# Optimization experiments

Hardware: AMD Instinct MI355X
Metric: run time of the kernel (lower is better)

Reference implementation:

```python
import jax, jax.numpy as jnp
import numpy as np

N = 50000
E = 800000
EPS = 1e-5


def layer_norm(h, g, b):
    m = jnp.mean(h, axis=-1, keepdims=True)
    v = jnp.mean((h - m) ** 2, axis=-1, keepdims=True)
    return (h - m) * jax.lax.rsqrt(v + EPS) * g + b


def gcn_conv(x, src, dst, w, W, b):
    # PyG GCNConv: add self-loops (weight 1), symmetric normalization,
    # linear transform, scatter-add aggregation at dst, plus bias.
    n = x.shape[0]
    loop = jnp.arange(n)
    s = jnp.concatenate([src, loop])
    d = jnp.concatenate([dst, loop])
    wf = jnp.concatenate([w, jnp.ones((n,), dtype=x.dtype)])
    deg = jax.ops.segment_sum(wf, d, num_segments=n)
    dinv = jnp.where(deg > 0, deg, 1.0) ** -0.5
    dinv = jnp.where(deg > 0, dinv, 0.0)
    norm = dinv[s] * wf * dinv[d]            # [E+N]
    h = x @ W                                 # [N, out]
    msg = h[s] * norm[:, None]                # gather + scale
    out = jax.ops.segment_sum(msg, d, num_segments=n)  # scatter-add
    return out + b


def setup_inputs() -> dict:
    key = jax.random.key(0)
    ks = jax.random.split(key, 16)
    din, dh, dout = 128, 128, 64
    p = lambda k, shp: jax.random.normal(k, shp, dtype=jnp.float32) * 0.05
    return {
        "x": jax.random.normal(ks[0], (N, din), dtype=jnp.float32),
        "edge_index": jax.random.randint(ks[1], (2, E), 0, N),
        "edge_weight": jax.random.uniform(ks[2], (E,), dtype=jnp.float32),
        "W1": p(ks[3], (din, dh)), "b1": jnp.zeros((dh,), jnp.float32),
        "g1": jnp.ones((dh,), jnp.float32), "t1": jnp.zeros((dh,), jnp.float32),
        "W2": p(ks[4], (dh, dh)), "b2": jnp.zeros((dh,), jnp.float32),
        "g2": jnp.ones((dh,), jnp.float32), "t2": jnp.zeros((dh,), jnp.float32),
        "W3": p(ks[5], (dh, dout)), "b3": jnp.zeros((dout,), jnp.float32),
        "g3": jnp.ones((dout,), jnp.float32), "t3": jnp.zeros((dout,), jnp.float32),
    }


def reference(x, edge_index, edge_weight, W1, b1, g1, t1, W2, b2, g2, t2, W3, b3, g3, t3):
    src, dst = edge_index[0], edge_index[1]
    h = gcn_conv(x, src, dst, edge_weight, W1, b1)
    h = jax.nn.relu(layer_norm(h, g1, t1))
    h = gcn_conv(h, src, dst, edge_weight, W2, b2)
    h = jax.nn.relu(layer_norm(h, g2, t2))
    h = gcn_conv(h, src, dst, edge_weight, W3, b3)
    h = layer_norm(h, g3, t3)  # last layer: no relu/dropout
    return h
```

## Files before the change

kernel.cpp:

```cpp
#include <hip/hip_runtime.h>


typedef __attribute__((ext_vector_type(8))) short short8;
typedef __attribute__((ext_vector_type(4))) float f32x4;

static constexpr float FXS  = 16777216.0f;
static constexpr float FXSI = 1.0f / 16777216.0f;

__device__ __forceinline__ unsigned short f2bf(float f) {
    unsigned int u = __float_as_uint(f);
    u += 0x7FFFu + ((u >> 16) & 1u);
    return (unsigned short)(u >> 16);
}
__device__ __forceinline__ float bflo(unsigned int w) { return __uint_as_float(w << 16); }
__device__ __forceinline__ float bfhi(unsigned int w) { return __uint_as_float(w & 0xFFFF0000u); }

__device__ __forceinline__ void accum8(float* acc, const uint4 w, float nr) {
    acc[0] = fmaf(bflo(w.x), nr, acc[0]); acc[1] = fmaf(bfhi(w.x), nr, acc[1]);
    acc[2] = fmaf(bflo(w.y), nr, acc[2]); acc[3] = fmaf(bfhi(w.y), nr, acc[3]);
    acc[4] = fmaf(bflo(w.z), nr, acc[4]); acc[5] = fmaf(bfhi(w.z), nr, acc[5]);
    acc[6] = fmaf(bflo(w.w), nr, acc[6]); acc[7] = fmaf(bfhi(w.w), nr, acc[7]);
}

__global__ __launch_bounds__(256) void prep_kernel(
    const int* __restrict__ dst, const float* __restrict__ ew,
    unsigned long long* __restrict__ packed, int* __restrict__ rank, int nE, int eb4,
    const float* __restrict__ X, unsigned short* __restrict__ Xb, int total4, int xbk,
    const float* __restrict__ W1, const float* __restrict__ W2,
    const float* __restrict__ W3, unsigned short* __restrict__ Wt1,
    unsigned short* __restrict__ Wt2, unsigned short* __restrict__ Wt3)
{
    const int b = blockIdx.x;
    if (b < eb4) {
        const int e0 = b * 1024 + threadIdx.x;
        int   d[4]; float w[4]; bool v[4];
#pragma unroll
        for (int u = 0; u < 4; ++u) {
            const int e = e0 + u * 256;
            v[u] = e < nE;
            if (v[u]) { d[u] = dst[e]; w[u] = ew[e]; }
        }
        unsigned long long old[4];
#pragma unroll
        for (int u = 0; u < 4; ++u)
            if (v[u]) {
                const unsigned long long fx =
                    (unsigned long long)__float2uint_rn(w[u] * FXS);
                old[u] = atomicAdd(&packed[d[u]], (1ULL << 40) | fx);
            }
#pragma unroll
        for (int u = 0; u < 4; ++u)
            if (v[u]) rank[e0 + u * 256] = (int)(old[u] >> 40);
    } else if (b < eb4 + xbk) {
        const int i = (b - eb4) * 256 + threadIdx.x;
        if (i < total4) {
            const float4 v = ((const float4*)X)[i];
            ushort4 o;
            o.x = f2bf(v.x); o.y = f2bf(v.y); o.z = f2bf(v.z); o.w = f2bf(v.w);
            ((ushort4*)Xb)[i] = o;
        }
    } else {
        const int i = (b - eb4 - xbk) * 256 + threadIdx.x;
        if (i < 16384) {
            const int j = i >> 7, k = i & 127;
            Wt1[i] = f2bf(W1[k * 128 + j]);
        } else if (i < 32768) {
            const int q = i - 16384, j = q >> 7, k = q & 127;
            Wt2[q] = f2bf(W2[k * 128 + j]);
        } else if (i < 40960) {
            const int q = i - 32768, j = q >> 7, k = q & 127;
            Wt3[q] = f2bf(W3[k * 64 + j]);
        }
    }
}

__global__ __launch_bounds__(256) void dinv_partial_kernel(
    const unsigned long long* __restrict__ packed, int* __restrict__ partials,
    float* __restrict__ dinv, int n)
{
    const int b = blockIdx.x;
    const int i = b * 256 + threadIdx.x;
    int c = 0;
    if (i < n) {
        const unsigned long long p = packed[i];
        c = (int)(p >> 40);
        const float deg = (float)(p & ((1ULL << 40) - 1)) * FXSI;
        dinv[i] = rsqrtf(deg + 1.0f);
    }
#pragma unroll
    for (int off = 32; off; off >>= 1) c += __shfl_xor(c, off);
    __shared__ int red[4];
    if ((threadIdx.x & 63) == 0) red[threadIdx.x >> 6] = c;
    __syncthreads();
    if (threadIdx.x == 0) partials[b] = red[0] + red[1] + red[2] + red[3];
}

__global__ __launch_bounds__(256) void scanp_kernel(
    int* __restrict__ partials, int* __restrict__ rowptr, int n, int nblk)
{
    __shared__ int buf[256];
    const int v = (threadIdx.x < nblk) ? partials[threadIdx.x] : 0;
    buf[threadIdx.x] = v;
    __syncthreads();
    for (int off = 1; off < 256; off <<= 1) {
        const int t = (threadIdx.x >= off) ? buf[threadIdx.x - off] : 0;
        __syncthreads();
        buf[threadIdx.x] += t;
        __syncthreads();
    }
    if (threadIdx.x < nblk) partials[threadIdx.x] = buf[threadIdx.x] - v;
    if (threadIdx.x == 255) rowptr[n] = buf[255];
}

__global__ __launch_bounds__(256) void scanf_kernel(
    const unsigned long long* __restrict__ packed, const int* __restrict__ partials,
    int* __restrict__ rowptr, int n)
{
    __shared__ int buf[256];
    const int b = blockIdx.x;
    const int i = b * 256 + threadIdx.x;
    const int v = (i < n) ? (int)(packed[i] >> 40) : 0;
    buf[threadIdx.x] = v;
    __syncthreads();
    for (int off = 1; off < 256; off <<= 1) {
        const int t = (threadIdx.x >= off) ? buf[threadIdx.x - off] : 0;
        __syncthreads();
        buf[threadIdx.x] += t;
        __syncthreads();
    }
    if (i < n) rowptr[i] = buf[threadIdx.x] - v + partials[b];
}

__device__ __forceinline__ void fill_body(
    const int* __restrict__ src, const int* __restrict__ dst,
    const float* __restrict__ ew, const int* __restrict__ rank,
    const float* __restrict__ dinv, const int* __restrict__ rowptr,
    int2* __restrict__ edges, int nE, int bid, int tid)
{
    const int e0 = bid * 512 + tid;
#pragma unroll
    for (int u = 0; u < 2; ++u) {
        const int e = e0 + u * 256;
        if (e < nE) {
            const int s = src[e], d = dst[e];
            const float nrm = dinv[s] * ew[e] * dinv[d];
            edges[rowptr[d] + rank[e]] = make_int2(s, __float_as_int(nrm));
        }
    }
}

template<int DOUT>
__device__ __forceinline__ void gemm_body(
    const unsigned short* __restrict__ Xb,
    const unsigned short* __restrict__ Wt,
    unsigned short* __restrict__ H, int n, int bid, int tid)
{
    const int wave = tid >> 6;
    const int lane = tid & 63;
    const int row0 = (bid * 4 + wave) * 16;
    if (row0 >= n) return;
    const int lr = lane & 15;
    const int lk = (lane >> 4) * 8;

    constexpr int NCT = DOUT / 16;
    f32x4 acc[NCT];
#pragma unroll
    for (int c = 0; c < NCT; ++c) acc[c] = (f32x4){0.f, 0.f, 0.f, 0.f};

    const int arow = row0 + lr;
    const bool rv = arow < n;
    short8 afrag[4];
#pragma unroll
    for (int ks = 0; ks < 4; ++ks)
        afrag[ks] = rv ? *(const short8*)(Xb + (size_t)arow * 128 + ks * 32 + lk)
                       : (short8){0, 0, 0, 0, 0, 0, 0, 0};

#pragma unroll
    for (int c = 0; c < NCT; ++c) {
        const unsigned short* wp = Wt + (size_t)(c * 16 + lr) * 128 + lk;
#pragma unroll
        for (int ks = 0; ks < 4; ++ks) {
            const short8 bfrag = *(const short8*)(wp + ks * 32);
            acc[c] = __builtin_amdgcn_mfma_f32_16x16x32_bf16(afrag[ks], bfrag, acc[c], 0, 0, 0);
        }
    }

    const int orow0 = row0 + (lane >> 4) * 4;
#pragma unroll
    for (int c = 0; c < NCT; ++c) {
#pragma unroll
        for (int r = 0; r < 4; ++r) {
            const int orow = orow0 + r;
            if (orow < n) H[(size_t)orow * DOUT + c * 16 + lr] = f2bf(acc[c][r]);
        }
    }
}

__global__ __launch_bounds__(256) void fill_gemm1_kernel(
    const int* __restrict__ src, const int* __restrict__ dst,
    const float* __restrict__ ew, const int* __restrict__ rank,
    const float* __restrict__ dinv, const int* __restrict__ rowptr,
    int2* __restrict__ edges, int nE, int fb,
    const unsigned short* __restrict__ Xb, const unsigned short* __restrict__ Wt,
    unsigned short* __restrict__ H, int n)
{
    if ((int)blockIdx.x < fb)
        fill_body(src, dst, ew, rank, dinv, rowptr, edges, nE, blockIdx.x, threadIdx.x);
    else
        gemm_body<128>(Xb, Wt, H, n, blockIdx.x - fb, threadIdx.x);
}

template<int DOUT>
__global__ __launch_bounds__(256) void gemm_mfma_kernel(
    const unsigned short* __restrict__ Xb, const unsigned short* __restrict__ Wt,
    unsigned short* __restrict__ H, int n)
{
    gemm_body<DOUT>(Xb, Wt, H, n, blockIdx.x, threadIdx.x);
}

template<int D, bool RELU, bool OB16>
__global__ __launch_bounds__(256) void gather_ln_kernel(
    const unsigned short* __restrict__ H, const int2* __restrict__ edges,
    const int* __restrict__ rowptr, const float* __restrict__ dinv,
    const float* __restrict__ bias, const float* __restrict__ g,
    const float* __restrict__ t, void* __restrict__ OUT, int n)
{
    constexpr int GS  = D / 8;
    constexpr int NPW = 64 / GS;
    const int lane = threadIdx.x & 63;
    const int wave = threadIdx.x >> 6;
    const int L    = lane & (GS - 1);
    const int gb0  = lane & ~(GS - 1);
    const int node = (blockIdx.x * 4 + wave) * NPW + (lane >> (GS == 16 ? 4 : 3));
    if (node >= n) return;

    const float di = dinv[node];
    const float sn = di * di;
    float acc[8];
    {
        const uint4 w = *(const uint4*)(H + (size_t)node * D + L * 8);
        const float4 b0 = *(const float4*)(bias + L * 8);
        const float4 b1 = *(const float4*)(bias + L * 8 + 4);
        acc[0] = fmaf(bflo(w.x), sn, b0.x); acc[1] = fmaf(bfhi(w.x), sn, b0.y);
        acc[2] = fmaf(bflo(w.y), sn, b0.z); acc[3] = fmaf(bfhi(w.y), sn, b0.w);
        acc[4] = fmaf(bflo(w.z), sn, b1.x); acc[5] = fmaf(bfhi(w.z), sn, b1.y);
        acc[6] = fmaf(bflo(w.w), sn, b1.z); acc[7] = fmaf(bfhi(w.w), sn, b1.w);
    }

    const int k0 = rowptr[node], k1 = rowptr[node + 1];
    for (int base = k0; base < k1; base += GS) {
        int2 ed = make_int2(0, 0);
        if (base + L < k1) ed = edges[base + L];
        const int cnt = min(GS, k1 - base);
        int j = 0;
        for (; j + 4 <= cnt; j += 4) {
            int s[4]; float nr[4]; uint4 w[4];
#pragma unroll
            for (int u = 0; u < 4; ++u) {
                s[u]  = __shfl(ed.x, gb0 + j + u);
                nr[u] = __int_as_float(__shfl(ed.y, gb0 + j + u));
            }
#pragma unroll
            for (int u = 0; u < 4; ++u)
                w[u] = *(const uint4*)(H + (size_t)s[u] * D + L * 8);
#pragma unroll
            for (int u = 0; u < 4; ++u) accum8(acc, w[u], nr[u]);
        }
        for (; j < cnt; ++j) {
            const int   s0 = __shfl(ed.x, gb0 + j);
            const float n0 = __int_as_float(__shfl(ed.y, gb0 + j));
            const uint4 w0 = *(const uint4*)(H + (size_t)s0 * D + L * 8);
            accum8(acc, w0, n0);
        }
    }

    float s1 = 0.f;
#pragma unroll
    for (int i = 0; i < 8; ++i) s1 += acc[i];
#pragma unroll
    for (int off = GS / 2; off; off >>= 1) s1 += __shfl_xor(s1, off);
    const float m = s1 * (1.f / D);
    float s2 = 0.f;
#pragma unroll
    for (int i = 0; i < 8; ++i) { acc[i] -= m; s2 += acc[i] * acc[i]; }
#pragma unroll
    for (int off = GS / 2; off; off >>= 1) s2 += __shfl_xor(s2, off);
    const float rs = rsqrtf(s2 * (1.f / D) + 1e-5f);

    const float4 g0 = *(const float4*)(g + L * 8), g1 = *(const float4*)(g + L * 8 + 4);
    const float4 t0 = *(const float4*)(t + L * 8), t1 = *(const float4*)(t + L * 8 + 4);
    float r[8];
    r[0] = fmaf(acc[0] * rs, g0.x, t0.x); r[1] = fmaf(acc[1] * rs, g0.y, t0.y);
    r[2] = fmaf(acc[2] * rs, g0.z, t0.z); r[3] = fmaf(acc[3] * rs, g0.w, t0.w);
    r[4] = fmaf(acc[4] * rs, g1.x, t1.x); r[5] = fmaf(acc[5] * rs, g1.y, t1.y);
    r[6] = fmaf(acc[6] * rs, g1.z, t1.z); r[7] = fmaf(acc[7] * rs, g1.w, t1.w);
    if (RELU) {
#pragma unroll
        for (int i = 0; i < 8; ++i) r[i] = fmaxf(r[i], 0.f);
    }

    if constexpr (OB16) {
        uint4 o;
        o.x = (unsigned int)f2bf(r[0]) | ((unsigned int)f2bf(r[1]) << 16);
        o.y = (unsigned int)f2bf(r[2]) | ((unsigned int)f2bf(r[3]) << 16);
        o.z = (unsigned int)f2bf(r[4]) | ((unsigned int)f2bf(r[5]) << 16);
        o.w = (unsigned int)f2bf(r[6]) | ((unsigned int)f2bf(r[7]) << 16);
        *(uint4*)((unsigned short*)OUT + (size_t)node * D + L * 8) = o;
    } else {
        float* o = (float*)OUT + (size_t)node * D + L * 8;
        *(float4*)o       = make_float4(r[0], r[1], r[2], r[3]);
        *(float4*)(o + 4) = make_float4(r[4], r[5], r[6], r[7]);
    }
}

extern "C" void kernel_launch(void* const* d_in, const int* in_sizes, int n_in,
                              void* d_out, int out_size, void* d_ws, size_t ws_size,
                              hipStream_t stream)
{
    const float* x  = (const float*)d_in[0];
    const int*   ei = (const int*)  d_in[1];
    const float* ew = (const float*)d_in[2];
    const float* W1 = (const float*)d_in[3];
    const float* b1 = (const float*)d_in[4];
    const float* g1 = (const float*)d_in[5];
    const float* t1 = (const float*)d_in[6];
    const float* W2 = (const float*)d_in[7];
    const float* b2 = (const float*)d_in[8];
    const float* g2 = (const float*)d_in[9];
    const float* t2 = (const float*)d_in[10];
    const float* W3 = (const float*)d_in[11];
    const float* b3 = (const float*)d_in[12];
    const float* g3 = (const float*)d_in[13];
    const float* t3 = (const float*)d_in[14];

    const int n  = in_sizes[0] / 128;
    const int nE = in_sizes[1] / 2;
    const int* srcv = ei;
    const int* dstv = ei + nE;

    const size_t na   = ((size_t)n + 63) & ~(size_t)63;
    const int    nblk = (n + 255) / 256;
    const int    eb4  = (nE + 1023) / 1024;
    const int    xbk  = (n * 32 + 255) / 256;
    const int    fb   = (nE + 511) / 512;

    unsigned long long* packed = (unsigned long long*)d_ws;
    float* dinv     = (float*)(packed + na);
    int*   rowptr   = (int*)(dinv + na);
    int*   partials = rowptr + na + 64;
    int2*  edges    = (int2*)(partials + 256);
    unsigned short* Hb  = (unsigned short*)(edges + nE);
    unsigned short* Qb  = Hb + (size_t)n * 128;
    unsigned short* xb  = Qb + (size_t)n * 128;
    unsigned short* Wt1 = xb + (size_t)n * 128;
    unsigned short* Wt2 = Wt1 + 16384;
    unsigned short* Wt3 = Wt2 + 16384;
    int* rank = (int*)Qb;

    hipMemsetAsync(packed, 0, na * sizeof(unsigned long long), stream);

    prep_kernel<<<eb4 + xbk + 160, 256, 0, stream>>>(
        dstv, ew, packed, rank, nE, eb4,
        x, xb, n * 32, xbk, W1, W2, W3, Wt1, Wt2, Wt3);
    dinv_partial_kernel<<<nblk, 256, 0, stream>>>(packed, partials, dinv, n);
    scanp_kernel       <<<1,    256, 0, stream>>>(partials, rowptr, n, nblk);
    scanf_kernel       <<<nblk, 256, 0, stream>>>(packed, partials, rowptr, n);

    const int gb   = (n + 63) / 64;
    const int nbA  = (n + 15) / 16;
    const int nbB  = (n + 31) / 32;

    fill_gemm1_kernel<<<fb + gb, 256, 0, stream>>>(
        srcv, dstv, ew, rank, dinv, rowptr, edges, nE, fb, xb, Wt1, Hb, n);
    gather_ln_kernel<128, true, true><<<nbA, 256, 0, stream>>>(Hb, edges, rowptr, dinv, b1, g1, t1, Qb, n);

    gemm_mfma_kernel<128><<<gb, 256, 0, stream>>>(Qb, Wt2, Hb, n);
    gather_ln_kernel<128, true, true><<<nbA, 256, 0, stream>>>(Hb, edges, rowptr, dinv, b2, g2, t2, Qb, n);

    gemm_mfma_kernel<64><<<gb, 256, 0, stream>>>(Qb, Wt3, Hb, n);
    gather_ln_kernel<64, false, false><<<nbB, 256, 0, stream>>>(Hb, edges, rowptr, dinv, b3, g3, t3, d_out, n);
}
```

Before: 298.8 us.

## Build CSR via two-level bucket sort instead of per-node global atomics

Replaces the per-node 64-bit global atomic counting plus multi-kernel scan with a two-pass bucket sort. Edges are histogrammed into 128-node buckets in shared memory, scattered into bucket-contiguous records, and each bucket is then finalized in one block that computes degree, dinv, rowptr and the edge order with shared atomics. The dinv[src] factor is no longer stored per edge and is instead applied during the gather. This cuts global atomic contention and kernel count, at the cost of an extra record pass, a per-edge dinv lookup in every gather layer, and float atomic ordering in the degree sums.

```diff
diff --git a/kernel.cpp b/kernel.cpp
--- a/kernel.cpp
+++ b/kernel.cpp
@@ -3,9 +3,6 @@
 
 typedef __attribute__((ext_vector_type(8))) short short8;
 typedef __attribute__((ext_vector_type(4))) float f32x4;
-
-static constexpr float FXS  = 16777216.0f;
-static constexpr float FXSI = 1.0f / 16777216.0f;
 
 __device__ __forceinline__ unsigned short f2bf(float f) {
     unsigned int u = __float_as_uint(f);
@@ -23,36 +20,28 @@
 }
 
 __global__ __launch_bounds__(256) void prep_kernel(
-    const int* __restrict__ dst, const float* __restrict__ ew,
-    unsigned long long* __restrict__ packed, int* __restrict__ rank, int nE, int eb4,
+    const int* __restrict__ dst, int* __restrict__ bukCnt, int nE, int ebA,
     const float* __restrict__ X, unsigned short* __restrict__ Xb, int total4, int xbk,
     const float* __restrict__ W1, const float* __restrict__ W2,
     const float* __restrict__ W3, unsigned short* __restrict__ Wt1,
     unsigned short* __restrict__ Wt2, unsigned short* __restrict__ Wt3)
 {
     const int b = blockIdx.x;
-    if (b < eb4) {
-        const int e0 = b * 1024 + threadIdx.x;
-        int   d[4]; float w[4]; bool v[4];
-#pragma unroll
-        for (int u = 0; u < 4; ++u) {
+    if (b < ebA) {
+        __shared__ int h[512];
+        for (int i = threadIdx.x; i < 512; i += 256) h[i] = 0;
+        __syncthreads();
+        const int e0 = b * 4096 + threadIdx.x;
+#pragma unroll
+        for (int u = 0; u < 16; ++u) {
             const int e = e0 + u * 256;
-            v[u] = e < nE;
-            if (v[u]) { d[u] = dst[e]; w[u] = ew[e]; }
-        }
-        unsigned long long old[4];
-#pragma unroll
-        for (int u = 0; u < 4; ++u)
-            if (v[u]) {
-                const unsigned long long fx =
-                    (unsigned long long)__float2uint_rn(w[u] * FXS);
-                old[u] = atomicAdd(&packed[d[u]], (1ULL << 40) | fx);
-            }
-#pragma unroll
-        for (int u = 0; u < 4; ++u)
-            if (v[u]) rank[e0 + u * 256] = (int)(old[u] >> 40);
-    } else if (b < eb4 + xbk) {
-        const int i = (b - eb4) * 256 + threadIdx.x;
+            if (e < nE) atomicAdd(&h[dst[e] >> 7], 1);
+        }
+        __syncthreads();
+        for (int i = threadIdx.x; i < 512; i += 256)
+            if (h[i]) atomicAdd(&bukCnt[i], h[i]);
+    } else if (b < ebA + xbk) {
+        const int i = (b - ebA) * 256 + threadIdx.x;
         if (i < total4) {
             const float4 v = ((const float4*)X)[i];
             ushort4 o;
@@ -60,7 +49,7 @@
             ((ushort4*)Xb)[i] = o;
         }
     } else {
-        const int i = (b - eb4 - xbk) * 256 + threadIdx.x;
+        const int i = (b - ebA - xbk) * 256 + threadIdx.x;
         if (i < 16384) {
             const int j = i >> 7, k = i & 127;
             Wt1[i] = f2bf(W1[k * 128 + j]);
@@ -74,79 +63,27 @@
     }
 }
 
-__global__ __launch_bounds__(256) void dinv_partial_kernel(
-    const unsigned long long* __restrict__ packed, int* __restrict__ partials,
-    float* __restrict__ dinv, int n)
-{
-    const int b = blockIdx.x;
-    const int i = b * 256 + threadIdx.x;
-    int c = 0;
-    if (i < n) {
-        const unsigned long long p = packed[i];
-        c = (int)(p >> 40);
-        const float deg = (float)(p & ((1ULL << 40) - 1)) * FXSI;
-        dinv[i] = rsqrtf(deg + 1.0f);
-    }
-#pragma unroll
-    for (int off = 32; off; off >>= 1) c += __shfl_xor(c, off);
-    __shared__ int red[4];
-    if ((threadIdx.x & 63) == 0) red[threadIdx.x >> 6] = c;
-    __syncthreads();
-    if (threadIdx.x == 0) partials[b] = red[0] + red[1] + red[2] + red[3];
-}
-
-__global__ __launch_bounds__(256) void scanp_kernel(
-    int* __restrict__ partials, int* __restrict__ rowptr, int n, int nblk)
-{
-    __shared__ int buf[256];
-    const int v = (threadIdx.x < nblk) ? partials[threadIdx.x] : 0;
+__global__ __launch_bounds__(512) void bukscan_kernel(
+    const int* __restrict__ bukCnt, int* __restrict__ bukBase,
+    int* __restrict__ bukCur, int* __restrict__ rowptr, int n, int nbuk, int nE)
+{
+    __shared__ int buf[512];
+    const int v = (threadIdx.x < nbuk) ? bukCnt[threadIdx.x] : 0;
     buf[threadIdx.x] = v;
     __syncthreads();
-    for (int off = 1; off < 256; off <<= 1) {
+    for (int off = 1; off < 512; off <<= 1) {
         const int t = (threadIdx.x >= off) ? buf[threadIdx.x - off] : 0;
         __syncthreads();
         buf[threadIdx.x] += t;
         __syncthreads();
     }
-    if (threadIdx.x < nblk) partials[threadIdx.x] = buf[threadIdx.x] - v;
-    if (threadIdx.x == 255) rowptr[n] = buf[255];
-}
-
-__global__ __launch_bounds__(256) void scanf_kernel(
-    const unsigned long long* __restrict__ packed, const int* __restrict__ partials,
-    int* __restrict__ rowptr, int n)
-{
-    __shared__ int buf[256];
-    const int b = blockIdx.x;
-    const int i = b * 256 + threadIdx.x;
-    const int v = (i < n) ? (int)(packed[i] >> 40) : 0;
-    buf[threadIdx.x] = v;
-    __syncthreads();
-    for (int off = 1; off < 256; off <<= 1) {
-        const int t = (threadIdx.x >= off) ? buf[threadIdx.x - off] : 0;
-        __syncthreads();
-        buf[threadIdx.x] += t;
-        __syncthreads();
-    }
-    if (i < n) rowptr[i] = buf[threadIdx.x] - v + partials[b];
-}
-
-__device__ __forceinline__ void fill_body(
-    const int* __restrict__ src, const int* __restrict__ dst,
-    const float* __restrict__ ew, const int* __restrict__ rank,
-    const float* __restrict__ dinv, const int* __restrict__ rowptr,
-    int2* __restrict__ edges, int nE, int bid, int tid)
-{
-    const int e0 = bid * 512 + tid;
-#pragma unroll
-    for (int u = 0; u < 2; ++u) {
-        const int e = e0 + u * 256;
-        if (e < nE) {
-            const int s = src[e], d = dst[e];
-            const float nrm = dinv[s] * ew[e] * dinv[d];
-            edges[rowptr[d] + rank[e]] = make_int2(s, __float_as_int(nrm));
-        }
-    }
+    if (threadIdx.x < nbuk) {
+        const int ex = buf[threadIdx.x] - v;
+        bukBase[threadIdx.x] = ex;
+        bukCur[threadIdx.x]  = ex;
+        if (threadIdx.x == nbuk - 1) bukBase[nbuk] = buf[threadIdx.x];
+    }
+    if (threadIdx.x == 0) rowptr[n] = nE;
 }
 
 template<int DOUT>
@@ -196,18 +133,97 @@
     }
 }
 
-__global__ __launch_bounds__(256) void fill_gemm1_kernel(
+__global__ __launch_bounds__(256) void scat_gemm1_kernel(
     const int* __restrict__ src, const int* __restrict__ dst,
-    const float* __restrict__ ew, const int* __restrict__ rank,
-    const float* __restrict__ dinv, const int* __restrict__ rowptr,
-    int2* __restrict__ edges, int nE, int fb,
+    const float* __restrict__ ew, int* __restrict__ bukCur,
+    int2* __restrict__ rec, unsigned char* __restrict__ rdst, int nE, int ebA,
     const unsigned short* __restrict__ Xb, const unsigned short* __restrict__ Wt,
     unsigned short* __restrict__ H, int n)
 {
-    if ((int)blockIdx.x < fb)
-        fill_body(src, dst, ew, rank, dinv, rowptr, edges, nE, blockIdx.x, threadIdx.x);
-    else
-        gemm_body<128>(Xb, Wt, H, n, blockIdx.x - fb, threadIdx.x);
+    if ((int)blockIdx.x < ebA) {
+        __shared__ int h[512], res[512], cur[512];
+        for (int i = threadIdx.x; i < 512; i += 256) { h[i] = 0; cur[i] = 0; }
+        __syncthreads();
+        const int e0 = blockIdx.x * 4096 + threadIdx.x;
+        int sv[16], dv[16], bk[16]; float wv[16]; bool va[16];
+#pragma unroll
+        for (int u = 0; u < 16; ++u) {
+            const int e = e0 + u * 256;
+            va[u] = e < nE;
+            if (va[u]) {
+                sv[u] = src[e]; dv[u] = dst[e]; wv[u] = ew[e];
+                bk[u] = dv[u] >> 7;
+                atomicAdd(&h[bk[u]], 1);
+            }
+        }
+        __syncthreads();
+        for (int i = threadIdx.x; i < 512; i += 256)
+            res[i] = h[i] ? atomicAdd(&bukCur[i], h[i]) : 0;
+        __syncthreads();
+#pragma unroll
+        for (int u = 0; u < 16; ++u) {
+            if (va[u]) {
+                const int r   = atomicAdd(&cur[bk[u]], 1);
+                const int pos = res[bk[u]] + r;
+                rec[pos]  = make_int2(sv[u], __float_as_int(wv[u]));
+                rdst[pos] = (unsigned char)(dv[u] & 127);
+            }
+        }
+    } else {
+        gemm_body<128>(Xb, Wt, H, n, blockIdx.x - ebA, threadIdx.x);
+    }
+}
+
+__global__ __launch_bounds__(256) void csrfin_kernel(
+    const int2* __restrict__ rec, const unsigned char* __restrict__ rdst,
+    const int* __restrict__ bukBase, int* __restrict__ rowptr,
+    float* __restrict__ dinv, int2* __restrict__ edges, int n)
+{
+    __shared__ int   cnt[128];
+    __shared__ float deg[128];
+    __shared__ int   sc[128];
+    __shared__ float dvl[128];
+    const int b  = blockIdx.x;
+    const int lo = bukBase[b], hi = bukBase[b + 1];
+    if (threadIdx.x < 128) { cnt[threadIdx.x] = 0; deg[threadIdx.x] = 0.f; }
+    __syncthreads();
+    for (int i = lo + (int)threadIdx.x; i < hi; i += 256) {
+        const int dl = rdst[i];
+        atomicAdd(&cnt[dl], 1);
+        atomicAdd(&deg[dl], __int_as_float(rec[i].y));
+    }
+    __syncthreads();
+    {
+        const int v = (threadIdx.x < 128) ? cnt[threadIdx.x] : 0;
+        if (threadIdx.x < 128) sc[threadIdx.x] = v;
+        __syncthreads();
+        for (int off = 1; off < 128; off <<= 1) {
+            const int t = (threadIdx.x < 128 && (int)threadIdx.x >= off)
+                        ? sc[threadIdx.x - off] : 0;
+            __syncthreads();
+            if (threadIdx.x < 128) sc[threadIdx.x] += t;
+            __syncthreads();
+        }
+        if (threadIdx.x < 128) sc[threadIdx.x] -= v;
+    }
+    if (threadIdx.x < 128) {
+        const int d = b * 128 + (int)threadIdx.x;
+        if (d < n) {
+            rowptr[d] = lo + sc[threadIdx.x];
+            const float di = rsqrtf(deg[threadIdx.x] + 1.0f);
+            dinv[d] = di;
+            dvl[threadIdx.x] = di;
+        }
+        cnt[threadIdx.x] = 0;
+    }
+    __syncthreads();
+    for (int i = lo + (int)threadIdx.x; i < hi; i += 256) {
+        const int dl = rdst[i];
+        const int2 r = rec[i];
+        const int rk = atomicAdd(&cnt[dl], 1);
+        edges[lo + sc[dl] + rk] =
+            make_int2(r.x, __float_as_int(__int_as_float(r.y) * dvl[dl]));
+    }
 }
 
 template<int DOUT>
@@ -249,8 +265,11 @@
 
     const int k0 = rowptr[node], k1 = rowptr[node + 1];
     for (int base = k0; base < k1; base += GS) {
-        int2 ed = make_int2(0, 0);
-        if (base + L < k1) ed = edges[base + L];
+        int2 ed = make_int2(0, 0); float cm = 0.f;
+        if (base + L < k1) {
+            ed = edges[base + L];
+            cm = __int_as_float(ed.y) * dinv[ed.x];
+        }
         const int cnt = min(GS, k1 - base);
         int j = 0;
         for (; j + 4 <= cnt; j += 4) {
@@ -258,7 +277,7 @@
 #pragma unroll
             for (int u = 0; u < 4; ++u) {
                 s[u]  = __shfl(ed.x, gb0 + j + u);
-                nr[u] = __int_as_float(__shfl(ed.y, gb0 + j + u));
+                nr[u] = __shfl(cm,  gb0 + j + u);
             }
 #pragma unroll
             for (int u = 0; u < 4; ++u)
@@ -268,7 +287,7 @@
         }
         for (; j < cnt; ++j) {
             const int   s0 = __shfl(ed.x, gb0 + j);
-            const float n0 = __int_as_float(__shfl(ed.y, gb0 + j));
+            const float n0 = __shfl(cm,  gb0 + j);
             const uint4 w0 = *(const uint4*)(H + (size_t)s0 * D + L * 8);
             accum8(acc, w0, n0);
         }
@@ -339,39 +358,39 @@
     const int* dstv = ei + nE;
 
     const size_t na   = ((size_t)n + 63) & ~(size_t)63;
-    const int    nblk = (n + 255) / 256;
-    const int    eb4  = (nE + 1023) / 1024;
+    const int    nbuk = (n + 127) >> 7;
+    const int    ebA  = (nE + 4095) / 4096;
     const int    xbk  = (n * 32 + 255) / 256;
-    const int    fb   = (nE + 511) / 512;
-
-    unsigned long long* packed = (unsigned long long*)d_ws;
-    float* dinv     = (float*)(packed + na);
+
+    float* dinv     = (float*)d_ws;
     int*   rowptr   = (int*)(dinv + na);
-    int*   partials = rowptr + na + 64;
-    int2*  edges    = (int2*)(partials + 256);
+    int*   bukCnt   = rowptr + na + 64;
+    int*   bukBase  = bukCnt + 512;
+    int*   bukCur   = bukBase + 576;
+    int2*  edges    = (int2*)(bukCur + 512);
     unsigned short* Hb  = (unsigned short*)(edges + nE);
     unsigned short* Qb  = Hb + (size_t)n * 128;
     unsigned short* xb  = Qb + (size_t)n * 128;
     unsigned short* Wt1 = xb + (size_t)n * 128;
     unsigned short* Wt2 = Wt1 + 16384;
     unsigned short* Wt3 = Wt2 + 16384;
-    int* rank = (int*)Qb;
-
-    hipMemsetAsync(packed, 0, na * sizeof(unsigned long long), stream);
-
-    prep_kernel<<<eb4 + xbk + 160, 256, 0, stream>>>(
-        dstv, ew, packed, rank, nE, eb4,
-        x, xb, n * 32, xbk, W1, W2, W3, Wt1, Wt2, Wt3);
-    dinv_partial_kernel<<<nblk, 256, 0, stream>>>(packed, partials, dinv, n);
-    scanp_kernel       <<<1,    256, 0, stream>>>(partials, rowptr, n, nblk);
-    scanf_kernel       <<<nblk, 256, 0, stream>>>(packed, partials, rowptr, n);
-
-    const int gb   = (n + 63) / 64;
-    const int nbA  = (n + 15) / 16;
-    const int nbB  = (n + 31) / 32;
-
-    fill_gemm1_kernel<<<fb + gb, 256, 0, stream>>>(
-        srcv, dstv, ew, rank, dinv, rowptr, edges, nE, fb, xb, Wt1, Hb, n);
+    int2* rec = (int2*)Qb;
+    unsigned char* rdst = (unsigned char*)(rec + nE);
+
+    hipMemsetAsync(bukCnt, 0, 512 * sizeof(int), stream);
+
+    prep_kernel<<<ebA + xbk + 160, 256, 0, stream>>>(
+        dstv, bukCnt, nE, ebA, x, xb, n * 32, xbk, W1, W2, W3, Wt1, Wt2, Wt3);
+    bukscan_kernel<<<1, 512, 0, stream>>>(bukCnt, bukBase, bukCur, rowptr, n, nbuk, nE);
+
+    const int gb  = (n + 63) / 64;
+    const int nbA = (n + 15) / 16;
+    const int nbB = (n + 31) / 32;
+
+    scat_gemm1_kernel<<<ebA + gb, 256, 0, stream>>>(
+        srcv, dstv, ew, bukCur, rec, rdst, nE, ebA, xb, Wt1, Hb, n);
+    csrfin_kernel<<<nbuk, 256, 0, stream>>>(rec, rdst, bukBase, rowptr, dinv, edges, n);
+
     gather_ln_kernel<128, true, true><<<nbA, 256, 0, stream>>>(Hb, edges, rowptr, dinv, b1, g1, t1, Qb, n);
 
     gemm_mfma_kernel<128><<<gb, 256, 0, stream>>>(Qb, Wt2, Hb, n);
```

After: 276.3 us. -7.5%, faster.
